# Kernel optimization log

Measured on AMD Instinct MI355X. Metric: run time of the kernel, lower is better.

## Reference

```python
import jax, jax.numpy as jnp
import numpy as np

B, W, F = 32, 128, 64      # batch, window (node feat dim), n_features (nodes)
H, D = 2, 128              # num_heads, out_window_size
NEG_SLOPE = 0.2


def setup_inputs() -> dict:
    key = jax.random.key(0)
    k1, k2, k3, k4, k5 = jax.random.split(key, 5)
    s = 1.0 / np.sqrt(W)
    return {
        "x": jax.random.normal(k1, (B, W, F), dtype=jnp.float32),
        "Wl": jax.random.normal(k2, (W, H * D), dtype=jnp.float32) * s,   # fc_src
        "Wr": jax.random.normal(k3, (W, H * D), dtype=jnp.float32) * s,   # fc_dst
        "attn_a": jax.random.normal(k4, (H, D), dtype=jnp.float32) * s,   # GATv2 attn vector
        "bias": jax.random.normal(k5, (H * D,), dtype=jnp.float32) * 0.01,
    }


def reference(x, Wl, Wr, attn_a, bias):
    """Dense batched GATv2 over a complete graph (with self loops) per batch.

    Matches DGL GATv2Conv (share_weights=False, bias=True, eval mode so
    feat_drop/attn_drop are identity), followed by mean over heads and the
    [B,F,D] -> [B,D,F] transpose of DGLFeatureGAT.forward.
    """
    # node features: x [B, W, F] -> [B, F, W]
    xn = jnp.swapaxes(x, 1, 2)
    el = jnp.einsum('bnw,whd->bnhd', xn, Wl.reshape(W, H, D))  # fc_src(h)
    er = jnp.einsum('bnw,whd->bnhd', xn, Wr.reshape(W, H, D))  # fc_dst(h)
    # edge (src=j -> dst=i): e_ij = a_h . LeakyReLU(el_j + er_i)
    pair = el[:, None, :, :, :] + er[:, :, None, :, :]          # [B, i, j, H, D]
    e = jnp.einsum('bijhd,hd->bhij', jax.nn.leaky_relu(pair, NEG_SLOPE), attn_a)
    # softmax over incoming edges (src j) per dst i
    alpha = jax.nn.softmax(e, axis=-1)                          # [B, H, i, j]
    rst = jnp.einsum('bhij,bjhd->bihd', alpha, el)              # aggregate fc_src feats
    rst = rst + bias.reshape(1, 1, H, D)
    out = rst.mean(axis=2)                                      # mean over heads -> [B, F, D]
    return jnp.swapaxes(out, 1, 2)                              # [B, D, F]
```

## Files before the change

kernel.cpp:

```cpp
#include <hip/hip_runtime.h>
#include <hip/hip_bf16.h>


constexpr int kB = 32, kW = 128, kF = 64, kH = 2, kD = 128, kHD = 256;
constexpr float kNeg = 0.2f;

__device__ __forceinline__ float lrelu(float v) { return fmaxf(v, kNeg * v); }

__global__ __launch_bounds__(512) void gat_proj(
    const float* __restrict__ x, const float* __restrict__ Wl,
    const float* __restrict__ Wr, float* __restrict__ elw,
    float* __restrict__ erw) {
  __shared__ float xw[kW][kF + 4];
  const int b = blockIdx.x >> 3;
  const int c0 = (blockIdx.x & 7) << 5;
  const int t = threadIdx.x;

  const float* xb = x + b * (kW * kF);
#pragma unroll
  for (int k = 0; k < 16; ++k) {
    const int idx = t + (k << 9);
    xw[idx >> 6][idx & 63] = xb[idx];
  }
  __syncthreads();

  const int c = c0 + (t & 31);
  const int n0 = (t >> 5) << 2;
  float accl[4] = {0.f, 0.f, 0.f, 0.f};
  float accr[4] = {0.f, 0.f, 0.f, 0.f};
  const float* wlp = Wl + c;
  const float* wrp = Wr + c;

#pragma unroll 8
  for (int w = 0; w < kW; ++w) {
    const float wl = wlp[w * kHD];
    const float wr = wrp[w * kHD];
    const float4 xa = *(const float4*)&xw[w][n0];
    accl[0] = fmaf(xa.x, wl, accl[0]); accr[0] = fmaf(xa.x, wr, accr[0]);
    accl[1] = fmaf(xa.y, wl, accl[1]); accr[1] = fmaf(xa.y, wr, accr[1]);
    accl[2] = fmaf(xa.z, wl, accl[2]); accr[2] = fmaf(xa.z, wr, accr[2]);
    accl[3] = fmaf(xa.w, wl, accl[3]); accr[3] = fmaf(xa.w, wr, accr[3]);
  }

  const int base = (b * kF + n0) * kHD + c;
#pragma unroll
  for (int k = 0; k < 4; ++k) {
    elw[base + k * kHD] = accl[k];
    erw[base + k * kHD] = accr[k];
  }
}

__global__ __launch_bounds__(512) void gat_attn(
    const float* __restrict__ elw, const float* __restrict__ erw,
    const float* __restrict__ attn_a, const float* __restrict__ bias,
    float* __restrict__ out) {
  __shared__ float el[kH][kF][kD + 4];
  __shared__ float er[kH][8][kD + 4];
  __shared__ float av[kH][kD];
  __shared__ float sAT[kH][kF][8];
  __shared__ float pbuf[4][kH][8][kD + 4];

  const int b = blockIdx.x >> 3;
  const int i0 = (blockIdx.x & 7) << 3;
  const int t = threadIdx.x;

  {
    const float* elb = elw + b * (kF * kHD);
#pragma unroll
    for (int k = 0; k < 8; ++k) {
      const int s = t + (k << 9);
      const int h = s >> 11;
      const int n = (s >> 5) & 63;
      const int dv = (s & 31) << 2;
      *(float4*)&el[h][n][dv] = *(const float4*)&elb[n * kHD + h * kD + dv];
    }
    const float* erb = erw + (b * kF + i0) * kHD;
    {
      const int h = t >> 8;
      const int r = (t >> 5) & 7;
      const int dv = (t & 31) << 2;
      *(float4*)&er[h][r][dv] = *(const float4*)&erb[r * kHD + h * kD + dv];
    }
    if (t < kH * kD) av[t >> 7][t & 127] = attn_a[t];
  }
  __syncthreads();

  {
    const int q = t & 15;
    const int jh = (t >> 4) & 1;
    const int i = (t >> 5) & 7;
    const int h = t >> 8;
    const int j0 = q + (jh << 5);
    const int j1 = j0 + 16;
    float e0 = 0.f, e1 = 0.f;
#pragma unroll
    for (int dv = 0; dv < kD; dv += 4) {
      const float4 rv = *(const float4*)&er[h][i][dv];
      const float4 a4 = *(const float4*)&av[h][dv];
      const float4 p0 = *(const float4*)&el[h][j0][dv];
      const float4 p1 = *(const float4*)&el[h][j1][dv];
      e0 = fmaf(lrelu(p0.x + rv.x), a4.x, e0);
      e0 = fmaf(lrelu(p0.y + rv.y), a4.y, e0);
      e0 = fmaf(lrelu(p0.z + rv.z), a4.z, e0);
      e0 = fmaf(lrelu(p0.w + rv.w), a4.w, e0);
      e1 = fmaf(lrelu(p1.x + rv.x), a4.x, e1);
      e1 = fmaf(lrelu(p1.y + rv.y), a4.y, e1);
      e1 = fmaf(lrelu(p1.z + rv.z), a4.z, e1);
      e1 = fmaf(lrelu(p1.w + rv.w), a4.w, e1);
    }
    float m = fmaxf(e0, e1);
#pragma unroll
    for (int off = 1; off < 32; off <<= 1) m = fmaxf(m, __shfl_xor(m, off));
    const float x0 = __expf(e0 - m);
    const float x1 = __expf(e1 - m);
    float s = x0 + x1;
#pragma unroll
    for (int off = 1; off < 32; off <<= 1) s += __shfl_xor(s, off);
    const float inv = 1.f / s;
    sAT[h][j0][i] = x0 * inv;
    sAT[h][j1][i] = x1 * inv;
  }
  __syncthreads();

  {
    const int dq = t & 31;
    const int ip = (t >> 5) & 1;
    const int jq = (t >> 6) & 3;
    const int h = t >> 8;
    float acc[4][4] = {};
    const int jbase = jq << 4;
#pragma unroll
    for (int jj = 0; jj < 16; ++jj) {
      const int j = jbase + jj;
      const float4 al = *(const float4*)&sAT[h][j][ip << 2];
      const float4 ev = *(const float4*)&el[h][j][dq << 2];
      acc[0][0] = fmaf(al.x, ev.x, acc[0][0]);
      acc[0][1] = fmaf(al.x, ev.y, acc[0][1]);
      acc[0][2] = fmaf(al.x, ev.z, acc[0][2]);
      acc[0][3] = fmaf(al.x, ev.w, acc[0][3]);
      acc[1][0] = fmaf(al.y, ev.x, acc[1][0]);
      acc[1][1] = fmaf(al.y, ev.y, acc[1][1]);
      acc[1][2] = fmaf(al.y, ev.z, acc[1][2]);
      acc[1][3] = fmaf(al.y, ev.w, acc[1][3]);
      acc[2][0] = fmaf(al.z, ev.x, acc[2][0]);
      acc[2][1] = fmaf(al.z, ev.y, acc[2][1]);
      acc[2][2] = fmaf(al.z, ev.z, acc[2][2]);
      acc[2][3] = fmaf(al.z, ev.w, acc[2][3]);
      acc[3][0] = fmaf(al.w, ev.x, acc[3][0]);
      acc[3][1] = fmaf(al.w, ev.y, acc[3][1]);
      acc[3][2] = fmaf(al.w, ev.z, acc[3][2]);
      acc[3][3] = fmaf(al.w, ev.w, acc[3][3]);
    }
#pragma unroll
    for (int ii = 0; ii < 4; ++ii) {
      float4 v;
      v.x = acc[ii][0]; v.y = acc[ii][1]; v.z = acc[ii][2]; v.w = acc[ii][3];
      *(float4*)&pbuf[jq][h][(ip << 2) + ii][dq << 2] = v;
    }
  }
  __syncthreads();

  {
    const int i = t & 7;
    const int d = (t >> 3) << 1;
    float o0 = 0.f, o1 = 0.f;
#pragma unroll
    for (int jq = 0; jq < 4; ++jq) {
#pragma unroll
      for (int h = 0; h < 2; ++h) {
        const float2 v = *(const float2*)&pbuf[jq][h][i][d];
        o0 += v.x;
        o1 += v.y;
      }
    }
    const float b0 = bias[d] + bias[kD + d];
    const float b1 = bias[d + 1] + bias[kD + d + 1];
    float* ob = out + b * (kD * kF) + i0 + i;
    ob[d * kF] = 0.5f * (o0 + b0);
    ob[(d + 1) * kF] = 0.5f * (o1 + b1);
  }
}

extern "C" void kernel_launch(void* const* d_in, const int* in_sizes, int n_in,
                              void* d_out, int out_size, void* d_ws,
                              size_t ws_size, hipStream_t stream) {
  (void)in_sizes; (void)n_in; (void)ws_size; (void)out_size;
  const float* x = (const float*)d_in[0];
  const float* Wl = (const float*)d_in[1];
  const float* Wr = (const float*)d_in[2];
  const float* attn_a = (const float*)d_in[3];
  const float* bias = (const float*)d_in[4];
  float* out = (float*)d_out;

  float* elw = (float*)d_ws;
  float* erw = elw + (size_t)kB * kF * kHD;

  gat_proj<<<dim3(kB * 8), dim3(512), 0, stream>>>(x, Wl, Wr, elw, erw);
  gat_attn<<<dim3(kB * 8), dim3(512), 0, stream>>>(elw, erw, attn_a, bias, out);
}
```

Measured before the change: 24.39 us.

## Fuse projection and attention kernels into one cooperative launch with grid sync

Merges the projection and attention kernels into a single cooperative kernel. The projection stage reuses the attention kernel's shared-memory el buffer as its staging area, and a grid-wide barrier separates the two stages. This removes the second launch and the gap between kernels. In exchange, 256 blocks of 512 threads must all be resident at once, the grid barrier has its own cost, and the fused kernel's larger shared-memory footprint may lower occupancy for the projection stage.

Result: slower. 67.87 us (+178.3%).

```diff
diff --git a/kernel.cpp b/kernel.cpp
--- a/kernel.cpp
+++ b/kernel.cpp
@@ -1,5 +1,8 @@
 #include <hip/hip_runtime.h>
 #include <hip/hip_bf16.h>
+#include <hip/hip_cooperative_groups.h>
+
+namespace cg = cooperative_groups;
 
 
 constexpr int kB = 32, kW = 128, kF = 64, kH = 2, kD = 128, kHD = 256;
@@ -7,52 +10,10 @@
 
 __device__ __forceinline__ float lrelu(float v) { return fmaxf(v, kNeg * v); }
 
-__global__ __launch_bounds__(512) void gat_proj(
+__global__ __launch_bounds__(512) void gat_coop(
     const float* __restrict__ x, const float* __restrict__ Wl,
-    const float* __restrict__ Wr, float* __restrict__ elw,
-    float* __restrict__ erw) {
-  __shared__ float xw[kW][kF + 4];
-  const int b = blockIdx.x >> 3;
-  const int c0 = (blockIdx.x & 7) << 5;
-  const int t = threadIdx.x;
-
-  const float* xb = x + b * (kW * kF);
-#pragma unroll
-  for (int k = 0; k < 16; ++k) {
-    const int idx = t + (k << 9);
-    xw[idx >> 6][idx & 63] = xb[idx];
-  }
-  __syncthreads();
-
-  const int c = c0 + (t & 31);
-  const int n0 = (t >> 5) << 2;
-  float accl[4] = {0.f, 0.f, 0.f, 0.f};
-  float accr[4] = {0.f, 0.f, 0.f, 0.f};
-  const float* wlp = Wl + c;
-  const float* wrp = Wr + c;
-
-#pragma unroll 8
-  for (int w = 0; w < kW; ++w) {
-    const float wl = wlp[w * kHD];
-    const float wr = wrp[w * kHD];
-    const float4 xa = *(const float4*)&xw[w][n0];
-    accl[0] = fmaf(xa.x, wl, accl[0]); accr[0] = fmaf(xa.x, wr, accr[0]);
-    accl[1] = fmaf(xa.y, wl, accl[1]); accr[1] = fmaf(xa.y, wr, accr[1]);
-    accl[2] = fmaf(xa.z, wl, accl[2]); accr[2] = fmaf(xa.z, wr, accr[2]);
-    accl[3] = fmaf(xa.w, wl, accl[3]); accr[3] = fmaf(xa.w, wr, accr[3]);
-  }
-
-  const int base = (b * kF + n0) * kHD + c;
-#pragma unroll
-  for (int k = 0; k < 4; ++k) {
-    elw[base + k * kHD] = accl[k];
-    erw[base + k * kHD] = accr[k];
-  }
-}
-
-__global__ __launch_bounds__(512) void gat_attn(
-    const float* __restrict__ elw, const float* __restrict__ erw,
-    const float* __restrict__ attn_a, const float* __restrict__ bias,
+    const float* __restrict__ Wr, const float* __restrict__ attn_a,
+    const float* __restrict__ bias, float* elw, float* erw,
     float* __restrict__ out) {
   __shared__ float el[kH][kF][kD + 4];
   __shared__ float er[kH][8][kD + 4];
@@ -60,9 +21,51 @@
   __shared__ float sAT[kH][kF][8];
   __shared__ float pbuf[4][kH][8][kD + 4];
 
-  const int b = blockIdx.x >> 3;
-  const int i0 = (blockIdx.x & 7) << 3;
+  const int bid = blockIdx.x;
   const int t = threadIdx.x;
+  const int b = bid >> 3;
+
+  {
+    float(*xw)[kF + 4] = reinterpret_cast<float(*)[kF + 4]>(&el[0][0][0]);
+    const int c0 = (bid & 7) << 5;
+
+    const float* xb = x + b * (kW * kF);
+#pragma unroll
+    for (int k = 0; k < 16; ++k) {
+      const int idx = t + (k << 9);
+      xw[idx >> 6][idx & 63] = xb[idx];
+    }
+    __syncthreads();
+
+    const int c = c0 + (t & 31);
+    const int n0 = (t >> 5) << 2;
+    float accl[4] = {0.f, 0.f, 0.f, 0.f};
+    float accr[4] = {0.f, 0.f, 0.f, 0.f};
+    const float* wlp = Wl + c;
+    const float* wrp = Wr + c;
+
+#pragma unroll 8
+    for (int w = 0; w < kW; ++w) {
+      const float wl = wlp[w * kHD];
+      const float wr = wrp[w * kHD];
+      const float4 xa = *(const float4*)&xw[w][n0];
+      accl[0] = fmaf(xa.x, wl, accl[0]); accr[0] = fmaf(xa.x, wr, accr[0]);
+      accl[1] = fmaf(xa.y, wl, accl[1]); accr[1] = fmaf(xa.y, wr, accr[1]);
+      accl[2] = fmaf(xa.z, wl, accl[2]); accr[2] = fmaf(xa.z, wr, accr[2]);
+      accl[3] = fmaf(xa.w, wl, accl[3]); accr[3] = fmaf(xa.w, wr, accr[3]);
+    }
+
+    const int base = (b * kF + n0) * kHD + c;
+#pragma unroll
+    for (int k = 0; k < 4; ++k) {
+      elw[base + k * kHD] = accl[k];
+      erw[base + k * kHD] = accr[k];
+    }
+  }
+
+  cg::this_grid().sync();
+
+  const int i0 = (bid & 7) << 3;
 
   {
     const float* elb = elw + b * (kF * kHD);
@@ -153,9 +156,8 @@
     }
 #pragma unroll
     for (int ii = 0; ii < 4; ++ii) {
-      float4 v;
-      v.x = acc[ii][0]; v.y = acc[ii][1]; v.z = acc[ii][2]; v.w = acc[ii][3];
-      *(float4*)&pbuf[jq][h][(ip << 2) + ii][dq << 2] = v;
+      *(float4*)&pbuf[jq][h][(ip << 2) + ii][dq << 2] =
+          make_float4(acc[ii][0], acc[ii][1], acc[ii][2], acc[ii][3]);
     }
   }
   __syncthreads();
@@ -195,6 +197,8 @@
   float* elw = (float*)d_ws;
   float* erw = elw + (size_t)kB * kF * kHD;
 
-  gat_proj<<<dim3(kB * 8), dim3(512), 0, stream>>>(x, Wl, Wr, elw, erw);
-  gat_attn<<<dim3(kB * 8), dim3(512), 0, stream>>>(elw, erw, attn_a, bias, out);
+  void* args[] = {(void*)&x,    (void*)&Wl,  (void*)&Wr, (void*)&attn_a,
+                  (void*)&bias, (void*)&elw, (void*)&erw, (void*)&out};
+  hipLaunchCooperativeKernel((const void*)gat_coop, dim3(kB * 8), dim3(512),
+                             args, 0, stream);
 }
```

## Fuse destination projection into attention kernel, dropping er workspace round-trip

Applied to the files above, without the earlier changes.

The first kernel now computes only the source projection (el). The attention kernel loads the batch's x tile into a shared buffer aliased with the partial-sum buffer and computes its own 8 rows of er from Wr on the spot. This removes half the projection work and the global write and read of er. In exchange, each attention block reloads the full x tile and streams all of Wr, which adds latency and a sync to that kernel.

Result: slower. 28.37 us (+16.3%).

```diff
diff --git a/kernel.cpp b/kernel.cpp
--- a/kernel.cpp
+++ b/kernel.cpp
@@ -7,10 +7,9 @@
 
 __device__ __forceinline__ float lrelu(float v) { return fmaxf(v, kNeg * v); }
 
-__global__ __launch_bounds__(512) void gat_proj(
+__global__ __launch_bounds__(512) void gat_proj_el(
     const float* __restrict__ x, const float* __restrict__ Wl,
-    const float* __restrict__ Wr, float* __restrict__ elw,
-    float* __restrict__ erw) {
+    float* __restrict__ elw) {
   __shared__ float xw[kW][kF + 4];
   const int b = blockIdx.x >> 3;
   const int c0 = (blockIdx.x & 7) << 5;
@@ -27,38 +26,35 @@
   const int c = c0 + (t & 31);
   const int n0 = (t >> 5) << 2;
   float accl[4] = {0.f, 0.f, 0.f, 0.f};
-  float accr[4] = {0.f, 0.f, 0.f, 0.f};
   const float* wlp = Wl + c;
-  const float* wrp = Wr + c;
 
 #pragma unroll 8
   for (int w = 0; w < kW; ++w) {
     const float wl = wlp[w * kHD];
-    const float wr = wrp[w * kHD];
     const float4 xa = *(const float4*)&xw[w][n0];
-    accl[0] = fmaf(xa.x, wl, accl[0]); accr[0] = fmaf(xa.x, wr, accr[0]);
-    accl[1] = fmaf(xa.y, wl, accl[1]); accr[1] = fmaf(xa.y, wr, accr[1]);
-    accl[2] = fmaf(xa.z, wl, accl[2]); accr[2] = fmaf(xa.z, wr, accr[2]);
-    accl[3] = fmaf(xa.w, wl, accl[3]); accr[3] = fmaf(xa.w, wr, accr[3]);
+    accl[0] = fmaf(xa.x, wl, accl[0]);
+    accl[1] = fmaf(xa.y, wl, accl[1]);
+    accl[2] = fmaf(xa.z, wl, accl[2]);
+    accl[3] = fmaf(xa.w, wl, accl[3]);
   }
 
   const int base = (b * kF + n0) * kHD + c;
 #pragma unroll
-  for (int k = 0; k < 4; ++k) {
-    elw[base + k * kHD] = accl[k];
-    erw[base + k * kHD] = accr[k];
-  }
+  for (int k = 0; k < 4; ++k) elw[base + k * kHD] = accl[k];
 }
 
+#define XW(w, n) u[(w) * 68 + (n)]
+#define PBUF(jq, h, i, d) u[(((jq) * 2 + (h)) * 8 + (i)) * 132 + (d)]
+
 __global__ __launch_bounds__(512) void gat_attn(
-    const float* __restrict__ elw, const float* __restrict__ erw,
-    const float* __restrict__ attn_a, const float* __restrict__ bias,
-    float* __restrict__ out) {
+    const float* __restrict__ elw, const float* __restrict__ x,
+    const float* __restrict__ Wr, const float* __restrict__ attn_a,
+    const float* __restrict__ bias, float* __restrict__ out) {
   __shared__ float el[kH][kF][kD + 4];
   __shared__ float er[kH][8][kD + 4];
   __shared__ float av[kH][kD];
   __shared__ float sAT[kH][kF][8];
-  __shared__ float pbuf[4][kH][8][kD + 4];
+  __shared__ float u[8704];
 
   const int b = blockIdx.x >> 3;
   const int i0 = (blockIdx.x & 7) << 3;
@@ -74,14 +70,32 @@
       const int dv = (s & 31) << 2;
       *(float4*)&el[h][n][dv] = *(const float4*)&elb[n * kHD + h * kD + dv];
     }
-    const float* erb = erw + (b * kF + i0) * kHD;
-    {
-      const int h = t >> 8;
-      const int r = (t >> 5) & 7;
-      const int dv = (t & 31) << 2;
-      *(float4*)&er[h][r][dv] = *(const float4*)&erb[r * kHD + h * kD + dv];
+    const float* xb = x + b * (kW * kF);
+#pragma unroll
+    for (int k = 0; k < 16; ++k) {
+      const int idx = t + (k << 9);
+      XW(idx >> 6, idx & 63) = xb[idx];
     }
     if (t < kH * kD) av[t >> 7][t & 127] = attn_a[t];
+  }
+  __syncthreads();
+
+  {
+    const int i = t >> 6;
+    const int c4 = (t & 63) << 2;
+    const int n = i0 + i;
+    float a[4] = {0.f, 0.f, 0.f, 0.f};
+    const float* wrp = Wr + c4;
+#pragma unroll 8
+    for (int w = 0; w < kW; ++w) {
+      const float xs = XW(w, n);
+      const float4 w4 = *(const float4*)&wrp[w * kHD];
+      a[0] = fmaf(xs, w4.x, a[0]);
+      a[1] = fmaf(xs, w4.y, a[1]);
+      a[2] = fmaf(xs, w4.z, a[2]);
+      a[3] = fmaf(xs, w4.w, a[3]);
+    }
+    *(float4*)&er[c4 >> 7][i][c4 & 127] = make_float4(a[0], a[1], a[2], a[3]);
   }
   __syncthreads();
 
@@ -153,9 +167,8 @@
     }
 #pragma unroll
     for (int ii = 0; ii < 4; ++ii) {
-      float4 v;
-      v.x = acc[ii][0]; v.y = acc[ii][1]; v.z = acc[ii][2]; v.w = acc[ii][3];
-      *(float4*)&pbuf[jq][h][(ip << 2) + ii][dq << 2] = v;
+      *(float4*)&PBUF(jq, h, (ip << 2) + ii, dq << 2) =
+          make_float4(acc[ii][0], acc[ii][1], acc[ii][2], acc[ii][3]);
     }
   }
   __syncthreads();
@@ -168,9 +181,9 @@
     for (int jq = 0; jq < 4; ++jq) {
 #pragma unroll
       for (int h = 0; h < 2; ++h) {
-        const float2 v = *(const float2*)&pbuf[jq][h][i][d];
-        o0 += v.x;
-        o1 += v.y;
+        const float* p = &PBUF(jq, h, i, d);
+        o0 += p[0];
+        o1 += p[1];
       }
     }
     const float b0 = bias[d] + bias[kD + d];
@@ -193,8 +206,8 @@
   float* out = (float*)d_out;
 
   float* elw = (float*)d_ws;
-  float* erw = elw + (size_t)kB * kF * kHD;
-
-  gat_proj<<<dim3(kB * 8), dim3(512), 0, stream>>>(x, Wl, Wr, elw, erw);
-  gat_attn<<<dim3(kB * 8), dim3(512), 0, stream>>>(elw, erw, attn_a, bias, out);
+
+  gat_proj_el<<<dim3(kB * 8), dim3(512), 0, stream>>>(x, Wl, elw);
+  gat_attn<<<dim3(kB * 8), dim3(512), 0, stream>>>(elw, x, Wr, attn_a, bias,
+                                                   out);
 }
```
